# Performance work log

Hardware: AMD Instinct MI355X
Metric: run time of the kernel (lower is better)

The kernel has to match this reference:

```python
import jax, jax.numpy as jnp
import numpy as np

B, T, H, I, O, R = 64, 1024, 1024, 8, 8, 4
NOISE_STD, ALPHA = 0.05, 0.2


def setup_inputs() -> dict:
    key = jax.random.key(0)
    ks = jax.random.split(key, 6)
    return {
        "x": jax.random.normal(ks[0], (B, T, I), jnp.float32),
        "noise": jax.random.normal(ks[1], (B, T, H), jnp.float32),
        "wi": jax.random.normal(ks[2], (I, H), jnp.float32),
        "si": jnp.ones((I,), jnp.float32),
        "m": jax.random.normal(ks[3], (H, R), jnp.float32),
        "n": jax.random.normal(ks[4], (H, R), jnp.float32),
        "b": jnp.zeros((H,), jnp.float32),
        "wo": jax.random.normal(ks[5], (H, O), jnp.float32) / H,
        "so": jnp.ones((O,), jnp.float32),
        "h0": jnp.zeros((H,), jnp.float32),
    }


def reference(x, noise, wi, si, m, n, b, wo, so, h0):
    hidden = h0.shape[0]
    batch = x.shape[0]
    wi_full = wi * si[:, None]          # (I, H): (wi.T * si).T
    wo_full = wo * so                   # (H, O)
    h_init = jnp.broadcast_to(h0, (batch, hidden))
    r_init = jnp.tanh(h_init)           # non_linearity(initial_states)
    # precompute input drive for all steps: (B,T,H) -> scan over time-major
    u = jnp.einsum('bti,ih->tbh', x, wi_full)
    noise_t = jnp.transpose(noise, (1, 0, 2))  # (T,B,H)

    def step(carry, inp):
        h, r = carry
        u_i, nz_i = inp
        rec = (r @ n) @ m.T / hidden                    # low-rank recurrence
        h = h + NOISE_STD * nz_i + ALPHA * (-h + rec + u_i)
        r = jnp.tanh(h + b)
        out = h @ wo_full                               # identity output nonlin
        return (h, r), out

    _, outs = jax.lax.scan(step, (h_init, r_init), (u, noise_t))
    return jnp.transpose(outs, (1, 0, 2))  # (B,T,O)
```

## Files before the change

kernel.cpp:

```cpp
#include <hip/hip_runtime.h>

#define BB 64
#define TT 1024
#define HH 1024
#define II 8
#define OO 8
#define RRK 4
#define NOISE_STD 0.05f
#define ALPHA 0.2f

template<int CTRL, int RM>
__device__ __forceinline__ float dpp_add(float acc, float src) {
    int s = __builtin_amdgcn_update_dpp(0, __float_as_int(src), CTRL, RM, 0xF, true);
    return acc + __int_as_float(s);
}

__device__ __forceinline__ float wave_sum(float x) {
    x = dpp_add<0xB1, 0xF>(x, x);
    x = dpp_add<0x4E, 0xF>(x, x);
    x = dpp_add<0x141, 0xF>(x, x);
    x = dpp_add<0x140, 0xF>(x, x);
    x = dpp_add<0x142, 0xA>(x, x);
    x = dpp_add<0x143, 0xC>(x, x);
    return x;
}

__device__ __forceinline__ float tanh_from_2x(float two_x) {
    float e = __expf(two_x);
    float r = __builtin_amdgcn_rcpf(e + 1.0f);
    return fmaf(-2.0f, r, 1.0f);
}

__device__ __forceinline__ void block_sync_lds() {
    asm volatile("s_waitcnt lgkmcnt(0)\n\ts_barrier" ::: "memory");
}

__global__ __launch_bounds__(256)
void prew_kernel(const float* __restrict__ noise, const float* __restrict__ wo,
                 const float* __restrict__ so, float* __restrict__ W) {
    __shared__ __align__(16) float red[4][4][8];

    const int tid  = threadIdx.x;
    const int wave = tid >> 6;
    const int lane = tid & 63;
    const int e0   = tid << 2;

    float woa[4][OO];
    {
        float so8[OO];
        #pragma unroll
        for (int o = 0; o < OO; ++o) so8[o] = so[o] * NOISE_STD;
        #pragma unroll
        for (int e = 0; e < 4; ++e) {
            const float4 a4 = *(const float4*)(wo + (e0 + e) * OO);
            const float4 b4 = *(const float4*)(wo + (e0 + e) * OO + 4);
            woa[e][0] = a4.x * so8[0]; woa[e][1] = a4.y * so8[1];
            woa[e][2] = a4.z * so8[2]; woa[e][3] = a4.w * so8[3];
            woa[e][4] = b4.x * so8[4]; woa[e][5] = b4.y * so8[5];
            woa[e][6] = b4.z * so8[6]; woa[e][7] = b4.w * so8[7];
        }
    }

    const int row0 = blockIdx.x * 32;
    for (int g = 0; g < 8; ++g) {
        #pragma unroll
        for (int j = 0; j < 4; ++j) {
            const int row = row0 + g * 4 + j;
            const float4 nz = *(const float4*)(noise + (size_t)row * HH + e0);
            float op[OO];
            #pragma unroll
            for (int o = 0; o < OO; ++o)
                op[o] = fmaf(nz.x, woa[0][o], fmaf(nz.y, woa[1][o],
                        fmaf(nz.z, woa[2][o], nz.w * woa[3][o])));
            #pragma unroll
            for (int o = 0; o < OO; ++o) op[o] = wave_sum(op[o]);
            if (lane == 63) {
                *(float4*)&red[j][wave][0] = make_float4(op[0], op[1], op[2], op[3]);
                *(float4*)&red[j][wave][4] = make_float4(op[4], op[5], op[6], op[7]);
            }
        }
        block_sync_lds();
        if (tid < 32) {
            const int j = tid >> 3, o = tid & 7;
            const int row = row0 + g * 4 + j;
            W[row * OO + o] = (red[j][0][o] + red[j][1][o]) +
                              (red[j][2][o] + red[j][3][o]);
        }
        block_sync_lds();
    }
}

__global__ __launch_bounds__(256, 1)
void rnn_seq_kernel(const float* __restrict__ x, const float* __restrict__ noise,
                    const float* __restrict__ wi, const float* __restrict__ si,
                    const float* __restrict__ mM, const float* __restrict__ nM,
                    const float* __restrict__ bv, const float* __restrict__ wo,
                    const float* __restrict__ so, const float* __restrict__ h0,
                    const float* __restrict__ W, float* __restrict__ out) {
    __shared__ __align__(16) float lds_x[TT * II];
    __shared__ __align__(16) float lds_W[TT * OO];
    __shared__ __align__(16) float lds_out[TT * OO];
    __shared__ __align__(16) float red[4][4][4];
    __shared__ __align__(16) float redc[4][104];
    __shared__ float ambx[104];

    const int tid  = threadIdx.x;
    const int b    = blockIdx.x;
    const int wave = tid >> 6;
    const int lane = tid & 63;
    const int e0   = tid << 2;
    const int oc   = tid & 7;

    {
        const float4* sx = (const float4*)(x + (size_t)b * (TT * II));
        const float4* sw = (const float4*)(W + (size_t)b * (TT * OO));
        float4* dx = (float4*)lds_x;
        float4* dw = (float4*)lds_W;
        #pragma unroll
        for (int k = 0; k < 8; ++k) {
            dx[k * 256 + tid] = sx[k * 256 + tid];
            dw[k * 256 + tid] = sw[k * 256 + tid];
        }
    }

    float wia[II][4];
    #pragma unroll
    for (int i = 0; i < II; ++i) {
        const float s  = ALPHA * si[i];
        const float4 w = *(const float4*)(wi + i * HH + e0);
        wia[i][0] = w.x * s; wia[i][1] = w.y * s; wia[i][2] = w.z * s; wia[i][3] = w.w * s;
    }
    float ma[4][RRK], nr[4][RRK];
    #pragma unroll
    for (int e = 0; e < 4; ++e) {
        const float4 m4 = *(const float4*)(mM + (e0 + e) * RRK);
        const float4 n4 = *(const float4*)(nM + (e0 + e) * RRK);
        const float cs = ALPHA / (float)HH;
        ma[e][0] = m4.x * cs; ma[e][1] = m4.y * cs; ma[e][2] = m4.z * cs; ma[e][3] = m4.w * cs;
        nr[e][0] = n4.x; nr[e][1] = n4.y; nr[e][2] = n4.z; nr[e][3] = n4.w;
    }
    float woa[4][OO];
    {
        float so8[OO];
        #pragma unroll
        for (int o = 0; o < OO; ++o) so8[o] = so[o];
        #pragma unroll
        for (int e = 0; e < 4; ++e) {
            const float4 a4 = *(const float4*)(wo + (e0 + e) * OO);
            const float4 b4 = *(const float4*)(wo + (e0 + e) * OO + 4);
            woa[e][0] = a4.x * so8[0]; woa[e][1] = a4.y * so8[1];
            woa[e][2] = a4.z * so8[2]; woa[e][3] = a4.w * so8[3];
            woa[e][4] = b4.x * so8[4]; woa[e][5] = b4.y * so8[5];
            woa[e][6] = b4.z * so8[6]; woa[e][7] = b4.w * so8[7];
        }
    }
    float tb2[4], h[4], r[4];
    {
        const float4 b4 = *(const float4*)(bv + e0);
        tb2[0] = 2.f * b4.x; tb2[1] = 2.f * b4.y; tb2[2] = 2.f * b4.z; tb2[3] = 2.f * b4.w;
        const float4 h4 = *(const float4*)(h0 + e0);
        h[0] = h4.x; h[1] = h4.y; h[2] = h4.z; h[3] = h4.w;
        #pragma unroll
        for (int e = 0; e < 4; ++e) r[e] = tanh_from_2x(2.f * h[e]);
    }

    #pragma unroll
    for (int kg = 0; kg < 26; ++kg) {
        float p[4];
        #pragma unroll
        for (int u = 0; u < 4; ++u) {
            const int k = kg * 4 + u;
            float s;
            if (k < 32) {
                const int q = k >> 3, o = k & 7;
                s = fmaf(ma[0][q], woa[0][o], fmaf(ma[1][q], woa[1][o],
                    fmaf(ma[2][q], woa[2][o], ma[3][q] * woa[3][o])));
            } else if (k < 96) {
                const int i = (k - 32) >> 3, o = k & 7;
                s = fmaf(wia[i][0], woa[0][o], fmaf(wia[i][1], woa[1][o],
                    fmaf(wia[i][2], woa[2][o], wia[i][3] * woa[3][o])));
            } else {
                const int o = k - 96;
                s = fmaf(h[0], woa[0][o], fmaf(h[1], woa[1][o],
                    fmaf(h[2], woa[2][o], h[3] * woa[3][o])));
            }
            p[u] = wave_sum(s);
        }
        if (lane == 63)
            *(float4*)&redc[wave][kg * 4] = make_float4(p[0], p[1], p[2], p[3]);
    }
    block_sync_lds();
    if (tid < 104)
        ambx[tid] = (redc[0][tid] + redc[1][tid]) + (redc[2][tid] + redc[3][tid]);
    __syncthreads();

    float Amr[RRK], Bxr[II], y;
    #pragma unroll
    for (int q = 0; q < RRK; ++q) Amr[q] = ambx[q * 8 + oc];
    #pragma unroll
    for (int i = 0; i < II; ++i) Bxr[i] = ambx[32 + i * 8 + oc];
    y = ambx[96 + oc];

    const float* nzp = noise + (size_t)b * (TT * HH) + e0;
    float4 nzb[4];
    #pragma unroll
    for (int j = 0; j < 4; ++j) nzb[j] = *(const float4*)(nzp + (size_t)j * HH);

    float4 xqc0 = *(const float4*)&lds_x[0];
    float4 xqc1 = *(const float4*)&lds_x[4];
    float  wqc  = lds_W[oc];

    for (int t0 = 0; t0 < TT; t0 += 4) {
        #pragma unroll
        for (int j = 0; j < 4; ++j) {
            const int t = t0 + j;

            const int tn = (t + 1 < TT) ? t + 1 : TT - 1;
            const float4 xqn0 = *(const float4*)&lds_x[tn * II];
            const float4 xqn1 = *(const float4*)&lds_x[tn * II + 4];
            const float  wqn  = lds_W[tn * OO + oc];

            float vp[RRK];
            #pragma unroll
            for (int q = 0; q < RRK; ++q)
                vp[q] = fmaf(r[0], nr[0][q], fmaf(r[1], nr[1][q],
                        fmaf(r[2], nr[2][q], r[3] * nr[3][q])));
            #pragma unroll
            for (int q = 0; q < RRK; ++q) vp[q] = wave_sum(vp[q]);
            if (lane == 63)
                *(float4*)&red[j][wave][0] = make_float4(vp[0], vp[1], vp[2], vp[3]);

            float ybase = fmaf(xqc0.x, Bxr[0], wqc);
            ybase = fmaf(xqc0.y, Bxr[1], ybase);
            ybase = fmaf(xqc0.z, Bxr[2], ybase);
            ybase = fmaf(xqc0.w, Bxr[3], ybase);
            ybase = fmaf(xqc1.x, Bxr[4], ybase);
            ybase = fmaf(xqc1.y, Bxr[5], ybase);
            ybase = fmaf(xqc1.z, Bxr[6], ybase);
            ybase = fmaf(xqc1.w, Bxr[7], ybase);

            float au[4];
            #pragma unroll
            for (int e = 0; e < 4; ++e) {
                float a = xqc0.x * wia[0][e];
                a = fmaf(xqc0.y, wia[1][e], a);
                a = fmaf(xqc0.z, wia[2][e], a);
                a = fmaf(xqc0.w, wia[3][e], a);
                a = fmaf(xqc1.x, wia[4][e], a);
                a = fmaf(xqc1.y, wia[5][e], a);
                a = fmaf(xqc1.z, wia[6][e], a);
                au[e] = fmaf(xqc1.w, wia[7][e], a);
            }

            block_sync_lds();

            const float4 s0 = *(const float4*)&red[j][0][0];
            const float4 s1 = *(const float4*)&red[j][1][0];
            const float4 s2 = *(const float4*)&red[j][2][0];
            const float4 s3 = *(const float4*)&red[j][3][0];
            const float v0 = (s0.x + s1.x) + (s2.x + s3.x);
            const float v1 = (s0.y + s1.y) + (s2.y + s3.y);
            const float v2 = (s0.z + s1.z) + (s2.z + s3.z);
            const float v3 = (s0.w + s1.w) + (s2.w + s3.w);

            const float nzv[4] = {nzb[j].x, nzb[j].y, nzb[j].z, nzb[j].w};
            #pragma unroll
            for (int e = 0; e < 4; ++e) {
                float acc = au[e];
                acc = fmaf(v0, ma[e][0], acc);
                acc = fmaf(v1, ma[e][1], acc);
                acc = fmaf(v2, ma[e][2], acc);
                acc = fmaf(v3, ma[e][3], acc);
                h[e] = fmaf(NOISE_STD, nzv[e], fmaf(1.0f - ALPHA, h[e], acc));
            }

            {
                float t4 = fmaf(v0, Amr[0], ybase);
                t4 = fmaf(v1, Amr[1], t4);
                t4 = fmaf(v2, Amr[2], t4);
                t4 = fmaf(v3, Amr[3], t4);
                y = fmaf(1.0f - ALPHA, y, t4);
                if (tid < OO) lds_out[t * OO + tid] = y;
            }

            {
                int tf = t + 4; if (tf >= TT) tf = 0;
                nzb[j] = *(const float4*)(nzp + (size_t)tf * HH);
            }

            #pragma unroll
            for (int e = 0; e < 4; ++e)
                r[e] = tanh_from_2x(fmaf(2.0f, h[e], tb2[e]));

            xqc0 = xqn0; xqc1 = xqn1; wqc = wqn;
        }
    }

    __syncthreads();
    {
        float4* dst = (float4*)(out + (size_t)b * (TT * OO));
        const float4* srcv = (const float4*)lds_out;
        #pragma unroll
        for (int k = 0; k < 8; ++k)
            dst[k * 256 + tid] = srcv[k * 256 + tid];
    }
}

extern "C" void kernel_launch(void* const* d_in, const int* in_sizes, int n_in,
                              void* d_out, int out_size, void* d_ws, size_t ws_size,
                              hipStream_t stream) {
    const float* x     = (const float*)d_in[0];
    const float* noise = (const float*)d_in[1];
    const float* wi    = (const float*)d_in[2];
    const float* si    = (const float*)d_in[3];
    const float* mM    = (const float*)d_in[4];
    const float* nM    = (const float*)d_in[5];
    const float* bv    = (const float*)d_in[6];
    const float* wo    = (const float*)d_in[7];
    const float* so    = (const float*)d_in[8];
    const float* h0    = (const float*)d_in[9];
    float* out = (float*)d_out;
    float* W   = (float*)d_ws;

    prew_kernel<<<dim3(2048), dim3(256), 0, stream>>>(noise, wo, so, W);
    rnn_seq_kernel<<<dim3(BB), dim3(256), 0, stream>>>(
        x, noise, wi, si, mM, nM, bv, wo, so, h0, W, out);
}
```

Measured before the change: 847.8 us.

## Fuse noise output projection into recurrent kernel and drop the pre-pass

Removes the separate pre-pass kernel that read the full noise tensor to compute its projection through the output weights. That projection is now computed inside the sequential kernel from the noise values it already loads each step, reduced across each wave with DPP, and staged in shared memory. The output update is delayed by one step so the cross-wave reduction completes under the next barrier. This saves a second full pass over the large noise tensor and one kernel launch, but adds eight wave reductions to every step of the latency-bound serial loop.

```diff
diff --git a/kernel.cpp b/kernel.cpp
--- a/kernel.cpp
+++ b/kernel.cpp
@@ -35,72 +35,17 @@
     asm volatile("s_waitcnt lgkmcnt(0)\n\ts_barrier" ::: "memory");
 }
 
-__global__ __launch_bounds__(256)
-void prew_kernel(const float* __restrict__ noise, const float* __restrict__ wo,
-                 const float* __restrict__ so, float* __restrict__ W) {
-    __shared__ __align__(16) float red[4][4][8];
-
-    const int tid  = threadIdx.x;
-    const int wave = tid >> 6;
-    const int lane = tid & 63;
-    const int e0   = tid << 2;
-
-    float woa[4][OO];
-    {
-        float so8[OO];
-        #pragma unroll
-        for (int o = 0; o < OO; ++o) so8[o] = so[o] * NOISE_STD;
-        #pragma unroll
-        for (int e = 0; e < 4; ++e) {
-            const float4 a4 = *(const float4*)(wo + (e0 + e) * OO);
-            const float4 b4 = *(const float4*)(wo + (e0 + e) * OO + 4);
-            woa[e][0] = a4.x * so8[0]; woa[e][1] = a4.y * so8[1];
-            woa[e][2] = a4.z * so8[2]; woa[e][3] = a4.w * so8[3];
-            woa[e][4] = b4.x * so8[4]; woa[e][5] = b4.y * so8[5];
-            woa[e][6] = b4.z * so8[6]; woa[e][7] = b4.w * so8[7];
-        }
-    }
-
-    const int row0 = blockIdx.x * 32;
-    for (int g = 0; g < 8; ++g) {
-        #pragma unroll
-        for (int j = 0; j < 4; ++j) {
-            const int row = row0 + g * 4 + j;
-            const float4 nz = *(const float4*)(noise + (size_t)row * HH + e0);
-            float op[OO];
-            #pragma unroll
-            for (int o = 0; o < OO; ++o)
-                op[o] = fmaf(nz.x, woa[0][o], fmaf(nz.y, woa[1][o],
-                        fmaf(nz.z, woa[2][o], nz.w * woa[3][o])));
-            #pragma unroll
-            for (int o = 0; o < OO; ++o) op[o] = wave_sum(op[o]);
-            if (lane == 63) {
-                *(float4*)&red[j][wave][0] = make_float4(op[0], op[1], op[2], op[3]);
-                *(float4*)&red[j][wave][4] = make_float4(op[4], op[5], op[6], op[7]);
-            }
-        }
-        block_sync_lds();
-        if (tid < 32) {
-            const int j = tid >> 3, o = tid & 7;
-            const int row = row0 + g * 4 + j;
-            W[row * OO + o] = (red[j][0][o] + red[j][1][o]) +
-                              (red[j][2][o] + red[j][3][o]);
-        }
-        block_sync_lds();
-    }
-}
-
 __global__ __launch_bounds__(256, 1)
 void rnn_seq_kernel(const float* __restrict__ x, const float* __restrict__ noise,
                     const float* __restrict__ wi, const float* __restrict__ si,
                     const float* __restrict__ mM, const float* __restrict__ nM,
                     const float* __restrict__ bv, const float* __restrict__ wo,
                     const float* __restrict__ so, const float* __restrict__ h0,
-                    const float* __restrict__ W, float* __restrict__ out) {
+                    float* __restrict__ out) {
     __shared__ __align__(16) float lds_x[TT * II];
-    __shared__ __align__(16) float lds_W[TT * OO];
     __shared__ __align__(16) float lds_out[TT * OO];
     __shared__ __align__(16) float red[4][4][4];
+    __shared__ __align__(16) float red_w[4][4][8];
     __shared__ __align__(16) float redc[4][104];
     __shared__ float ambx[104];
 
@@ -113,14 +58,10 @@
 
     {
         const float4* sx = (const float4*)(x + (size_t)b * (TT * II));
-        const float4* sw = (const float4*)(W + (size_t)b * (TT * OO));
         float4* dx = (float4*)lds_x;
-        float4* dw = (float4*)lds_W;
-        #pragma unroll
-        for (int k = 0; k < 8; ++k) {
+        #pragma unroll
+        for (int k = 0; k < 8; ++k)
             dx[k * 256 + tid] = sx[k * 256 + tid];
-            dw[k * 256 + tid] = sw[k * 256 + tid];
-        }
     }
 
     float wia[II][4];
@@ -208,7 +149,8 @@
 
     float4 xqc0 = *(const float4*)&lds_x[0];
     float4 xqc1 = *(const float4*)&lds_x[4];
-    float  wqc  = lds_W[oc];
+
+    float pv0 = 0.f, pv1 = 0.f, pv2 = 0.f, pv3 = 0.f, pyb = 0.f;
 
     for (int t0 = 0; t0 < TT; t0 += 4) {
         #pragma unroll
@@ -218,7 +160,6 @@
             const int tn = (t + 1 < TT) ? t + 1 : TT - 1;
             const float4 xqn0 = *(const float4*)&lds_x[tn * II];
             const float4 xqn1 = *(const float4*)&lds_x[tn * II + 4];
-            const float  wqn  = lds_W[tn * OO + oc];
 
             float vp[RRK];
             #pragma unroll
@@ -230,7 +171,7 @@
             if (lane == 63)
                 *(float4*)&red[j][wave][0] = make_float4(vp[0], vp[1], vp[2], vp[3]);
 
-            float ybase = fmaf(xqc0.x, Bxr[0], wqc);
+            float ybase = xqc0.x * Bxr[0];
             ybase = fmaf(xqc0.y, Bxr[1], ybase);
             ybase = fmaf(xqc0.z, Bxr[2], ybase);
             ybase = fmaf(xqc0.w, Bxr[3], ybase);
@@ -253,11 +194,32 @@
             }
 
             block_sync_lds();
+            __builtin_amdgcn_sched_barrier(0);
 
             const float4 s0 = *(const float4*)&red[j][0][0];
             const float4 s1 = *(const float4*)&red[j][1][0];
             const float4 s2 = *(const float4*)&red[j][2][0];
             const float4 s3 = *(const float4*)&red[j][3][0];
+            const int jp = (j + 3) & 3;
+            const float wr0 = red_w[jp][0][oc];
+            const float wr1 = red_w[jp][1][oc];
+            const float wr2 = red_w[jp][2][oc];
+            const float wr3 = red_w[jp][3][oc];
+
+            {
+                float wp[OO];
+                #pragma unroll
+                for (int o = 0; o < OO; ++o)
+                    wp[o] = fmaf(nzb[j].x, woa[0][o], fmaf(nzb[j].y, woa[1][o],
+                            fmaf(nzb[j].z, woa[2][o], nzb[j].w * woa[3][o])));
+                #pragma unroll
+                for (int o = 0; o < OO; ++o) wp[o] = wave_sum(wp[o]);
+                if (lane == 63) {
+                    *(float4*)&red_w[j][wave][0] = make_float4(wp[0], wp[1], wp[2], wp[3]);
+                    *(float4*)&red_w[j][wave][4] = make_float4(wp[4], wp[5], wp[6], wp[7]);
+                }
+            }
+
             const float v0 = (s0.x + s1.x) + (s2.x + s3.x);
             const float v1 = (s0.y + s1.y) + (s2.y + s3.y);
             const float v2 = (s0.z + s1.z) + (s2.z + s3.z);
@@ -274,13 +236,15 @@
                 h[e] = fmaf(NOISE_STD, nzv[e], fmaf(1.0f - ALPHA, h[e], acc));
             }
 
-            {
-                float t4 = fmaf(v0, Amr[0], ybase);
-                t4 = fmaf(v1, Amr[1], t4);
-                t4 = fmaf(v2, Amr[2], t4);
-                t4 = fmaf(v3, Amr[3], t4);
+            if (t > 0) {
+                const float wr = (wr0 + wr1) + (wr2 + wr3);
+                float t4 = fmaf(NOISE_STD, wr, pyb);
+                t4 = fmaf(pv0, Amr[0], t4);
+                t4 = fmaf(pv1, Amr[1], t4);
+                t4 = fmaf(pv2, Amr[2], t4);
+                t4 = fmaf(pv3, Amr[3], t4);
                 y = fmaf(1.0f - ALPHA, y, t4);
-                if (tid < OO) lds_out[t * OO + tid] = y;
+                if (tid < OO) lds_out[(t - 1) * OO + tid] = y;
             }
 
             {
@@ -292,8 +256,22 @@
             for (int e = 0; e < 4; ++e)
                 r[e] = tanh_from_2x(fmaf(2.0f, h[e], tb2[e]));
 
-            xqc0 = xqn0; xqc1 = xqn1; wqc = wqn;
+            xqc0 = xqn0; xqc1 = xqn1;
+            pv0 = v0; pv1 = v1; pv2 = v2; pv3 = v3; pyb = ybase;
         }
+    }
+
+    block_sync_lds();
+    {
+        const float wr = (red_w[3][0][oc] + red_w[3][1][oc]) +
+                         (red_w[3][2][oc] + red_w[3][3][oc]);
+        float t4 = fmaf(NOISE_STD, wr, pyb);
+        t4 = fmaf(pv0, Amr[0], t4);
+        t4 = fmaf(pv1, Amr[1], t4);
+        t4 = fmaf(pv2, Amr[2], t4);
+        t4 = fmaf(pv3, Amr[3], t4);
+        y = fmaf(1.0f - ALPHA, y, t4);
+        if (tid < OO) lds_out[(TT - 1) * OO + tid] = y;
     }
 
     __syncthreads();
@@ -320,9 +298,7 @@
     const float* so    = (const float*)d_in[8];
     const float* h0    = (const float*)d_in[9];
     float* out = (float*)d_out;
-    float* W   = (float*)d_ws;
-
-    prew_kernel<<<dim3(2048), dim3(256), 0, stream>>>(noise, wo, so, W);
+
     rnn_seq_kernel<<<dim3(BB), dim3(256), 0, stream>>>(
-        x, noise, wi, si, mM, nM, bv, wo, so, h0, W, out);
-}
+        x, noise, wi, si, mM, nM, bv, wo, so, h0, out);
+}
```

New measurement: 1.028 ms. 21.3% more time.
